# Kernel tuning notes

Hardware: AMD Instinct MI355X
Metric: run time of the kernel (lower is better)

The kernel has to match this reference:

```python
import jax, jax.numpy as jnp
import numpy as np

B, A, H, V, L = 8192, 128, 256, 64, 20


def setup_inputs() -> dict:
    key = jax.random.key(0)
    ks = jax.random.split(key, 9)
    s = lambda k, sh: jax.random.normal(k, sh, dtype=jnp.float32) * 0.05
    return {
        "attrVector": jax.random.normal(ks[0], (B, A), dtype=jnp.float32),
        "W_a": s(ks[1], (H, A)), "b_a": s(ks[2], (H,)),
        "W_ih": s(ks[3], (4 * H, V)), "W_hh": s(ks[4], (4 * H, H)),
        "b_ih": s(ks[5], (4 * H,)), "b_hh": s(ks[6], (4 * H,)),
        "W_v": s(ks[7], (V, H)), "b_v": s(ks[8], (V,)),
    }


def _lstm_step(x, h, c, W_ih, W_hh, b_ih, b_hh):
    # PyTorch LSTM gate order: input, forget, cell(g), output
    gates = x @ W_ih.T + b_ih + h @ W_hh.T + b_hh  # [B, 4H]
    i, f, g, o = jnp.split(gates, 4, axis=-1)
    c_new = jax.nn.sigmoid(f) * c + jax.nn.sigmoid(i) * jnp.tanh(g)
    h_new = jax.nn.sigmoid(o) * jnp.tanh(c_new)
    return h_new, c_new


def reference(attrVector, W_a, b_a, W_ih, W_hh, b_ih, b_hh, W_v, b_v):
    batch = attrVector.shape[0]
    dt = attrVector.dtype
    # attr2hidden -> initial hidden state; cell state zeros (init_hidden)
    h = attrVector @ W_a.T + b_a                      # [B, H]
    c = jnp.zeros_like(h)
    # start-token step (all-zeros embedding)
    x0 = jnp.zeros((batch, V), dtype=dt)
    h, c = _lstm_step(x0, h, c, W_ih, W_hh, b_ih, b_hh)

    keys = jax.random.split(jax.random.key(42), L)

    def step(carry, k):
        h, c, slp, plp, ep = carry
        logits = h @ W_v.T + b_v                      # [B, V]
        logp = jax.nn.log_softmax(logits, axis=-1)
        plp = plp + jnp.sum(jnp.exp(logp) * logp, axis=-1)  # negative entropy
        ch = jax.random.categorical(k, logits, axis=-1)     # [B] int sample
        lp = jnp.take_along_axis(logp, ch[:, None], axis=-1)[:, 0]
        slp = slp + lp
        ep = ep * jnp.exp(lp)
        x = jax.nn.one_hot(ch, V, dtype=dt)
        h2, c2 = _lstm_step(x, h, c, W_ih, W_hh, b_ih, b_hh)
        return (h2, c2, slp, plp, ep), ch

    zeros = jnp.zeros((batch,), dtype=dt)
    ones = jnp.ones((batch,), dtype=dt)
    (_, _, slp, plp, ep), msgs = jax.lax.scan(step, (h, c, zeros, zeros, ones), keys)
    message = msgs.T.astype(jnp.int64) if msgs.dtype != jnp.int64 else msgs.T  # [B, L]
    return message, slp, plp, ep
```

## Files before the change

kernel.cpp:

```cpp
#include <hip/hip_runtime.h>
#include <stdint.h>

#define BATCH 8192
#define ADIM 128
#define HDIM 256
#define VDIM 64
#define NSTEP 20
#define TB 16
#define HSP 17
#define ASP 20

typedef union { float4 v; float f[4]; } F4;

__device__ __forceinline__ uint32_t rotl32(uint32_t x, uint32_t d) {
  return (x << d) | (x >> (32u - d));
}
__device__ __forceinline__ void tf4(uint32_t& x0, uint32_t& x1, int r0, int r1, int r2, int r3) {
  x0 += x1; x1 = rotl32(x1, r0); x1 ^= x0;
  x0 += x1; x1 = rotl32(x1, r1); x1 ^= x0;
  x0 += x1; x1 = rotl32(x1, r2); x1 ^= x0;
  x0 += x1; x1 = rotl32(x1, r3); x1 ^= x0;
}
__device__ __forceinline__ void threefry2x32(uint32_t k0, uint32_t k1, uint32_t x0, uint32_t x1,
                                             uint32_t& o0, uint32_t& o1) {
  uint32_t k2 = k0 ^ k1 ^ 0x1BD11BDAu;
  x0 += k0; x1 += k1;
  tf4(x0, x1, 13, 15, 26, 6);  x0 += k1; x1 += k2 + 1u;
  tf4(x0, x1, 17, 29, 16, 24); x0 += k2; x1 += k0 + 2u;
  tf4(x0, x1, 13, 15, 26, 6);  x0 += k0; x1 += k1 + 3u;
  tf4(x0, x1, 17, 29, 16, 24); x0 += k1; x1 += k2 + 4u;
  tf4(x0, x1, 13, 15, 26, 6);  x0 += k2; x1 += k0 + 5u;
  o0 = x0; o1 = x1;
}

__device__ __forceinline__ float sigm(float x) { return 1.0f / (1.0f + expf(-x)); }

__device__ __forceinline__ float bcast(float x, int t) {
  return __int_as_float(__builtin_amdgcn_readlane(__float_as_int(x), t));
}

__global__ void prep_kernel(const float* __restrict__ Whh, const float* __restrict__ Wv,
                            const float* __restrict__ Wa, const float* __restrict__ Wih,
                            float* __restrict__ ws) {
  int n = blockIdx.x * blockDim.x + threadIdx.x;
  int stride = gridDim.x * blockDim.x;
  float* WhhT4 = ws;
  float* WvT   = ws + 262144;
  float* WaT   = ws + 278528;
  float* WihT4 = ws + 311296;
  for (int i = n; i < 256 * 1024; i += stride) {
    int k = i >> 10, rem = i & 1023, u = rem >> 2, g = rem & 3;
    WhhT4[i] = Whh[((g << 8) + u) * 256 + k];
  }
  for (int i = n; i < 256 * 64; i += stride) { int k = i >> 6, v = i & 63; WvT[i] = Wv[v * 256 + k]; }
  for (int i = n; i < 128 * 256; i += stride) { int k = i >> 8, u = i & 255; WaT[i] = Wa[u * 128 + k]; }
  for (int i = n; i < 64 * 1024; i += stride) {
    int v = i >> 10, rem = i & 1023, u = rem >> 2, g = rem & 3;
    WihT4[i] = Wih[((g << 8) + u) * 64 + v];
  }
}

__global__ __launch_bounds__(256, 2) void sender_main(
    const float* __restrict__ attr, const float* __restrict__ b_a,
    const float* __restrict__ b_ih, const float* __restrict__ b_hh,
    const float* __restrict__ b_v,
    const float* __restrict__ WhhT4, const float* __restrict__ WvT,
    const float* __restrict__ WaT, const float* __restrict__ WihT4,
    float* __restrict__ out) {
  __shared__ float h_s[HDIM][HSP];
  __shared__ __align__(16) float attr_s[ADIM][ASP];
  __shared__ float slp_s[TB], plp_s[TB], ep_s[TB];
  __shared__ int ch_s[TB];

  const int tid = threadIdx.x;
  const int w = tid >> 6;
  const int lane = tid & 63;
  const int u = (w << 6) + lane;
  const int w4 = w << 2;
  const int b0 = blockIdx.x * TB;

  if (tid < TB) { slp_s[tid] = 0.0f; plp_s[tid] = 0.0f; ep_s[tid] = 1.0f; }

  {
    int r = tid >> 5;
    int cm = (tid & 31) << 2;
    #pragma unroll
    for (int pass = 0; pass < 2; ++pass) {
      int row = r + (pass << 3);
      F4 vv; vv.v = *(const float4*)&attr[(size_t)(b0 + row) * ADIM + cm];
      attr_s[cm + 0][row] = vv.f[0];
      attr_s[cm + 1][row] = vv.f[1];
      attr_s[cm + 2][row] = vv.f[2];
      attr_s[cm + 3][row] = vv.f[3];
    }
  }
  __syncthreads();

  {
    float acc[16];
    #pragma unroll
    for (int s = 0; s < 16; ++s) acc[s] = 0.0f;
    #pragma unroll 2
    for (int k = 0; k < ADIM; ++k) {
      F4 a0, a1, a2, a3;
      a0.v = *(const float4*)&attr_s[k][0];
      a1.v = *(const float4*)&attr_s[k][4];
      a2.v = *(const float4*)&attr_s[k][8];
      a3.v = *(const float4*)&attr_s[k][12];
      float wa = WaT[(k << 8) + u];
      #pragma unroll
      for (int j = 0; j < 4; ++j) {
        acc[j]      = fmaf(a0.f[j], wa, acc[j]);
        acc[4 + j]  = fmaf(a1.f[j], wa, acc[4 + j]);
        acc[8 + j]  = fmaf(a2.f[j], wa, acc[8 + j]);
        acc[12 + j] = fmaf(a3.f[j], wa, acc[12 + j]);
      }
    }
    float ba = b_a[u];
    #pragma unroll
    for (int s = 0; s < 16; ++s) h_s[u][s] = acc[s] + ba;
  }
  __syncthreads();

  float c_r[16];
  #pragma unroll
  for (int s = 0; s < 16; ++s) c_r[s] = 0.0f;

  float bg[4];
  #pragma unroll
  for (int g = 0; g < 4; ++g) bg[g] = b_ih[(g << 8) + u] + b_hh[(g << 8) + u];
  const float bv = b_v[lane];

  {
    float ga[16][4];
    #pragma unroll
    for (int s = 0; s < 16; ++s)
      #pragma unroll
      for (int g = 0; g < 4; ++g) ga[s][g] = 0.0f;
    #pragma unroll 1
    for (int kc = 0; kc < 16; ++kc) {
      const int k0 = kc << 4;
      const int kk = k0 + (lane & 15);
      float hch[16];
      #pragma unroll
      for (int s = 0; s < 16; ++s) hch[s] = h_s[kk][(s + w4) & 15];
      #pragma unroll
      for (int t = 0; t < 16; ++t) {
        const int k = k0 + t;
        F4 wv4; wv4.v = *(const float4*)&WhhT4[(k << 10) + (u << 2)];
        #pragma unroll
        for (int s = 0; s < 16; ++s) {
          float hb = bcast(hch[s], t);
          ga[s][0] = fmaf(hb, wv4.f[0], ga[s][0]);
          ga[s][1] = fmaf(hb, wv4.f[1], ga[s][1]);
          ga[s][2] = fmaf(hb, wv4.f[2], ga[s][2]);
          ga[s][3] = fmaf(hb, wv4.f[3], ga[s][3]);
        }
      }
    }
    __syncthreads();
    float hn[16];
    #pragma unroll
    for (int s = 0; s < 16; ++s) {
      float gi = ga[s][0] + bg[0];
      float gf = ga[s][1] + bg[1];
      float gg = ga[s][2] + bg[2];
      float go = ga[s][3] + bg[3];
      float cn = sigm(gf) * c_r[s] + sigm(gi) * tanhf(gg);
      hn[s] = sigm(go) * tanhf(cn);
      c_r[s] = cn;
    }
    #pragma unroll
    for (int s = 0; s < 16; ++s) h_s[u][(s + w4) & 15] = hn[s];
    __syncthreads();
  }

  #pragma unroll 1
  for (int l = 0; l < NSTEP; ++l) {
    uint32_t kl0, kl1;
    threefry2x32(0u, 42u, 0u, (uint32_t)l, kl0, kl1);

    const bool last = (l == NSTEP - 1);
    float la[4] = {0.0f, 0.0f, 0.0f, 0.0f};
    float ga[16][4];
    #pragma unroll
    for (int s = 0; s < 16; ++s)
      #pragma unroll
      for (int g = 0; g < 4; ++g) ga[s][g] = 0.0f;

    if (!last) {
      #pragma unroll 1
      for (int kc = 0; kc < 16; ++kc) {
        const int k0 = kc << 4;
        const int kk = k0 + (lane & 15);
        float hch[16];
        #pragma unroll
        for (int s = 0; s < 16; ++s) hch[s] = h_s[kk][(s + w4) & 15];
        #pragma unroll
        for (int t = 0; t < 16; ++t) {
          const int k = k0 + t;
          F4 wv4; wv4.v = *(const float4*)&WhhT4[(k << 10) + (u << 2)];
          float wvv = WvT[(k << 6) | lane];
          #pragma unroll
          for (int s = 0; s < 16; ++s) {
            float hb = bcast(hch[s], t);
            if (s < 4) la[s] = fmaf(hb, wvv, la[s]);
            ga[s][0] = fmaf(hb, wv4.f[0], ga[s][0]);
            ga[s][1] = fmaf(hb, wv4.f[1], ga[s][1]);
            ga[s][2] = fmaf(hb, wv4.f[2], ga[s][2]);
            ga[s][3] = fmaf(hb, wv4.f[3], ga[s][3]);
          }
        }
      }
    } else {
      #pragma unroll 1
      for (int kc = 0; kc < 16; ++kc) {
        const int k0 = kc << 4;
        const int kk = k0 + (lane & 15);
        float hch[4];
        #pragma unroll
        for (int s = 0; s < 4; ++s) hch[s] = h_s[kk][(s + w4) & 15];
        #pragma unroll
        for (int t = 0; t < 16; ++t) {
          const int k = k0 + t;
          float wvv = WvT[(k << 6) | lane];
          #pragma unroll
          for (int s = 0; s < 4; ++s) la[s] = fmaf(bcast(hch[s], t), wvv, la[s]);
        }
      }
    }

    #pragma unroll
    for (int db = 0; db < 4; ++db) {
      float x = la[db] + bv;
      float m = x;
      #pragma unroll
      for (int o = 32; o > 0; o >>= 1) m = fmaxf(m, __shfl_xor(m, o));
      float e = expf(x - m);
      float s = e;
      #pragma unroll
      for (int o = 32; o > 0; o >>= 1) s += __shfl_xor(s, o);
      float lse = logf(s);
      float logp = x - m - lse;
      float p = expf(logp);
      float pe = p * logp;
      #pragma unroll
      for (int o = 32; o > 0; o >>= 1) pe += __shfl_xor(pe, o);
      uint32_t idx = ((uint32_t)(b0 + w4 + db) << 6) | (uint32_t)lane;
      uint32_t r0, r1;
      threefry2x32(kl0, kl1, 0u, idx, r0, r1);
      uint32_t bits = r0 ^ r1;
      float f01 = __uint_as_float((bits >> 9) | 0x3f800000u) - 1.0f;
      const float TINY = 1.17549435e-38f;
      float uu2 = fmaxf(TINY, f01 + TINY);
      float gn = -logf(-logf(uu2));
      float y = gn + x;
      float by = y; int bi = lane;
      #pragma unroll
      for (int o = 32; o > 0; o >>= 1) {
        float oy = __shfl_xor(by, o);
        int oi = __shfl_xor(bi, o);
        if (oy > by || (oy == by && oi < bi)) { by = oy; bi = oi; }
      }
      float lp = __shfl(logp, bi, 64);
      if (lane == 0) {
        int bb = w4 + db;
        ch_s[bb] = bi;
        slp_s[bb] += lp;
        plp_s[bb] += pe;
        ep_s[bb] *= expf(lp);
        out[(size_t)(b0 + bb) * NSTEP + l] = (float)bi;
      }
    }

    if (!last) {
      __syncthreads();
      float hn[16];
      #pragma unroll
      for (int s = 0; s < 16; ++s) {
        const int sp = (s + w4) & 15;
        F4 wi; wi.v = *(const float4*)&WihT4[(ch_s[sp] << 10) + (u << 2)];
        float gi = ga[s][0] + wi.f[0] + bg[0];
        float gf = ga[s][1] + wi.f[1] + bg[1];
        float gg = ga[s][2] + wi.f[2] + bg[2];
        float go = ga[s][3] + wi.f[3] + bg[3];
        float cn = sigm(gf) * c_r[s] + sigm(gi) * tanhf(gg);
        hn[s] = sigm(go) * tanhf(cn);
        c_r[s] = cn;
      }
      #pragma unroll
      for (int s = 0; s < 16; ++s) h_s[u][(s + w4) & 15] = hn[s];
      __syncthreads();
    }
  }

  __syncthreads();
  if (tid < TB) {
    int bb = b0 + tid;
    out[(size_t)BATCH * NSTEP + bb]             = slp_s[tid];
    out[(size_t)BATCH * NSTEP + BATCH + bb]     = plp_s[tid];
    out[(size_t)BATCH * NSTEP + 2 * BATCH + bb] = ep_s[tid];
  }
}

extern "C" void kernel_launch(void* const* d_in, const int* in_sizes, int n_in,
                              void* d_out, int out_size, void* d_ws, size_t ws_size,
                              hipStream_t stream) {
  const float* attr = (const float*)d_in[0];
  const float* W_a  = (const float*)d_in[1];
  const float* b_a  = (const float*)d_in[2];
  const float* W_ih = (const float*)d_in[3];
  const float* W_hh = (const float*)d_in[4];
  const float* b_ih = (const float*)d_in[5];
  const float* b_hh = (const float*)d_in[6];
  const float* W_v  = (const float*)d_in[7];
  const float* b_v  = (const float*)d_in[8];
  float* ws = (float*)d_ws;

  prep_kernel<<<256, 256, 0, stream>>>(W_hh, W_v, W_a, W_ih, ws);
  sender_main<<<BATCH / TB, 256, 0, stream>>>(
      attr, b_a, b_ih, b_hh, b_v,
      ws, ws + 262144, ws + 278528, ws + 311296,
      (float*)d_out);
}
```

Baseline: 1.441 ms.

## Retile LSTM gate work so each lane computes two hidden units over eight samples

The per-wave split changes from 64 hidden units × 16 samples to 128 hidden units (two per lane) × 8 samples. This halves the LDS reads of h and the cross-lane broadcasts per FMA group, which were a large share of the inner-loop cost. In exchange, each block now reads W_hh and W_ih from global/L2 twice as often, since two waves share each weight column. The rotated sample ordering keeps the logit samples aligned with the existing w4 mapping.

```diff
diff --git a/kernel.cpp b/kernel.cpp
--- a/kernel.cpp
+++ b/kernel.cpp
@@ -75,7 +75,12 @@
   const int tid = threadIdx.x;
   const int w = tid >> 6;
   const int lane = tid & 63;
-  const int u = (w << 6) + lane;
+  const int half = w & 1;
+  const int sh = w >> 1;
+  const int u_a = (half << 7) + lane;
+  const int u_b = u_a + 64;
+  const int base = sh << 3;
+  const int rot = half << 2;
   const int w4 = w << 2;
   const int b0 = blockIdx.x * TB;
 
@@ -97,81 +102,108 @@
   __syncthreads();
 
   {
-    float acc[16];
-    #pragma unroll
-    for (int s = 0; s < 16; ++s) acc[s] = 0.0f;
+    float acc[2][8];
+    #pragma unroll
+    for (int c = 0; c < 2; ++c)
+      #pragma unroll
+      for (int p = 0; p < 8; ++p) acc[c][p] = 0.0f;
     #pragma unroll 2
     for (int k = 0; k < ADIM; ++k) {
-      F4 a0, a1, a2, a3;
-      a0.v = *(const float4*)&attr_s[k][0];
-      a1.v = *(const float4*)&attr_s[k][4];
-      a2.v = *(const float4*)&attr_s[k][8];
-      a3.v = *(const float4*)&attr_s[k][12];
-      float wa = WaT[(k << 8) + u];
-      #pragma unroll
-      for (int j = 0; j < 4; ++j) {
-        acc[j]      = fmaf(a0.f[j], wa, acc[j]);
-        acc[4 + j]  = fmaf(a1.f[j], wa, acc[4 + j]);
-        acc[8 + j]  = fmaf(a2.f[j], wa, acc[8 + j]);
-        acc[12 + j] = fmaf(a3.f[j], wa, acc[12 + j]);
-      }
-    }
-    float ba = b_a[u];
-    #pragma unroll
-    for (int s = 0; s < 16; ++s) h_s[u][s] = acc[s] + ba;
+      F4 lo, hi;
+      lo.v = *(const float4*)&attr_s[k][base];
+      hi.v = *(const float4*)&attr_s[k][base + 4];
+      float wa_a = WaT[(k << 8) + u_a];
+      float wa_b = WaT[(k << 8) + u_b];
+      #pragma unroll
+      for (int p = 0; p < 8; ++p) {
+        float av = (p < 4) ? lo.f[p] : hi.f[p - 4];
+        acc[0][p] = fmaf(av, wa_a, acc[0][p]);
+        acc[1][p] = fmaf(av, wa_b, acc[1][p]);
+      }
+    }
+    float ba_a = b_a[u_a], ba_b = b_a[u_b];
+    #pragma unroll
+    for (int p = 0; p < 8; ++p) {
+      h_s[u_a][base + p] = acc[0][p] + ba_a;
+      h_s[u_b][base + p] = acc[1][p] + ba_b;
+    }
   }
   __syncthreads();
 
-  float c_r[16];
+  float c_r[2][8];
   #pragma unroll
-  for (int s = 0; s < 16; ++s) c_r[s] = 0.0f;
-
-  float bg[4];
+  for (int c = 0; c < 2; ++c)
+    #pragma unroll
+    for (int s = 0; s < 8; ++s) c_r[c][s] = 0.0f;
+
+  float bga[4], bgb[4];
   #pragma unroll
-  for (int g = 0; g < 4; ++g) bg[g] = b_ih[(g << 8) + u] + b_hh[(g << 8) + u];
+  for (int g = 0; g < 4; ++g) {
+    bga[g] = b_ih[(g << 8) + u_a] + b_hh[(g << 8) + u_a];
+    bgb[g] = b_ih[(g << 8) + u_b] + b_hh[(g << 8) + u_b];
+  }
   const float bv = b_v[lane];
 
   {
-    float ga[16][4];
-    #pragma unroll
-    for (int s = 0; s < 16; ++s)
-      #pragma unroll
-      for (int g = 0; g < 4; ++g) ga[s][g] = 0.0f;
+    float ga[2][8][4];
+    #pragma unroll
+    for (int c = 0; c < 2; ++c)
+      #pragma unroll
+      for (int s = 0; s < 8; ++s)
+        #pragma unroll
+        for (int g = 0; g < 4; ++g) ga[c][s][g] = 0.0f;
     #pragma unroll 1
     for (int kc = 0; kc < 16; ++kc) {
       const int k0 = kc << 4;
       const int kk = k0 + (lane & 15);
-      float hch[16];
-      #pragma unroll
-      for (int s = 0; s < 16; ++s) hch[s] = h_s[kk][(s + w4) & 15];
+      float hch[8];
+      #pragma unroll
+      for (int s = 0; s < 8; ++s) hch[s] = h_s[kk][base + ((s + rot) & 7)];
       #pragma unroll
       for (int t = 0; t < 16; ++t) {
         const int k = k0 + t;
-        F4 wv4; wv4.v = *(const float4*)&WhhT4[(k << 10) + (u << 2)];
-        #pragma unroll
-        for (int s = 0; s < 16; ++s) {
+        F4 wa, wb;
+        wa.v = *(const float4*)&WhhT4[(k << 10) + (u_a << 2)];
+        wb.v = *(const float4*)&WhhT4[(k << 10) + (u_b << 2)];
+        #pragma unroll
+        for (int s = 0; s < 8; ++s) {
           float hb = bcast(hch[s], t);
-          ga[s][0] = fmaf(hb, wv4.f[0], ga[s][0]);
-          ga[s][1] = fmaf(hb, wv4.f[1], ga[s][1]);
-          ga[s][2] = fmaf(hb, wv4.f[2], ga[s][2]);
-          ga[s][3] = fmaf(hb, wv4.f[3], ga[s][3]);
+          ga[0][s][0] = fmaf(hb, wa.f[0], ga[0][s][0]);
+          ga[0][s][1] = fmaf(hb, wa.f[1], ga[0][s][1]);
+          ga[0][s][2] = fmaf(hb, wa.f[2], ga[0][s][2]);
+          ga[0][s][3] = fmaf(hb, wa.f[3], ga[0][s][3]);
+          ga[1][s][0] = fmaf(hb, wb.f[0], ga[1][s][0]);
+          ga[1][s][1] = fmaf(hb, wb.f[1], ga[1][s][1]);
+          ga[1][s][2] = fmaf(hb, wb.f[2], ga[1][s][2]);
+          ga[1][s][3] = fmaf(hb, wb.f[3], ga[1][s][3]);
         }
       }
     }
     __syncthreads();
-    float hn[16];
-    #pragma unroll
-    for (int s = 0; s < 16; ++s) {
-      float gi = ga[s][0] + bg[0];
-      float gf = ga[s][1] + bg[1];
-      float gg = ga[s][2] + bg[2];
-      float go = ga[s][3] + bg[3];
-      float cn = sigm(gf) * c_r[s] + sigm(gi) * tanhf(gg);
-      hn[s] = sigm(go) * tanhf(cn);
-      c_r[s] = cn;
-    }
-    #pragma unroll
-    for (int s = 0; s < 16; ++s) h_s[u][(s + w4) & 15] = hn[s];
+    #pragma unroll
+    for (int s = 0; s < 8; ++s) {
+      const int p = base + ((s + rot) & 7);
+      {
+        float gi = ga[0][s][0] + bga[0];
+        float gf = ga[0][s][1] + bga[1];
+        float gg = ga[0][s][2] + bga[2];
+        float go = ga[0][s][3] + bga[3];
+        float cn = sigm(gf) * c_r[0][s] + sigm(gi) * tanhf(gg);
+        float hn = sigm(go) * tanhf(cn);
+        c_r[0][s] = cn;
+        h_s[u_a][p] = hn;
+      }
+      {
+        float gi = ga[1][s][0] + bgb[0];
+        float gf = ga[1][s][1] + bgb[1];
+        float gg = ga[1][s][2] + bgb[2];
+        float go = ga[1][s][3] + bgb[3];
+        float cn = sigm(gf) * c_r[1][s] + sigm(gi) * tanhf(gg);
+        float hn = sigm(go) * tanhf(cn);
+        c_r[1][s] = cn;
+        h_s[u_b][p] = hn;
+      }
+    }
     __syncthreads();
   }
 
@@ -182,33 +214,41 @@
 
     const bool last = (l == NSTEP - 1);
     float la[4] = {0.0f, 0.0f, 0.0f, 0.0f};
-    float ga[16][4];
-    #pragma unroll
-    for (int s = 0; s < 16; ++s)
-      #pragma unroll
-      for (int g = 0; g < 4; ++g) ga[s][g] = 0.0f;
+    float ga[2][8][4];
+    #pragma unroll
+    for (int c = 0; c < 2; ++c)
+      #pragma unroll
+      for (int s = 0; s < 8; ++s)
+        #pragma unroll
+        for (int g = 0; g < 4; ++g) ga[c][s][g] = 0.0f;
 
     if (!last) {
       #pragma unroll 1
       for (int kc = 0; kc < 16; ++kc) {
         const int k0 = kc << 4;
         const int kk = k0 + (lane & 15);
-        float hch[16];
-        #pragma unroll
-        for (int s = 0; s < 16; ++s) hch[s] = h_s[kk][(s + w4) & 15];
+        float hch[8];
+        #pragma unroll
+        for (int s = 0; s < 8; ++s) hch[s] = h_s[kk][base + ((s + rot) & 7)];
         #pragma unroll
         for (int t = 0; t < 16; ++t) {
           const int k = k0 + t;
-          F4 wv4; wv4.v = *(const float4*)&WhhT4[(k << 10) + (u << 2)];
+          F4 wa, wb;
+          wa.v = *(const float4*)&WhhT4[(k << 10) + (u_a << 2)];
+          wb.v = *(const float4*)&WhhT4[(k << 10) + (u_b << 2)];
           float wvv = WvT[(k << 6) | lane];
           #pragma unroll
-          for (int s = 0; s < 16; ++s) {
+          for (int s = 0; s < 8; ++s) {
             float hb = bcast(hch[s], t);
             if (s < 4) la[s] = fmaf(hb, wvv, la[s]);
-            ga[s][0] = fmaf(hb, wv4.f[0], ga[s][0]);
-            ga[s][1] = fmaf(hb, wv4.f[1], ga[s][1]);
-            ga[s][2] = fmaf(hb, wv4.f[2], ga[s][2]);
-            ga[s][3] = fmaf(hb, wv4.f[3], ga[s][3]);
+            ga[0][s][0] = fmaf(hb, wa.f[0], ga[0][s][0]);
+            ga[0][s][1] = fmaf(hb, wa.f[1], ga[0][s][1]);
+            ga[0][s][2] = fmaf(hb, wa.f[2], ga[0][s][2]);
+            ga[0][s][3] = fmaf(hb, wa.f[3], ga[0][s][3]);
+            ga[1][s][0] = fmaf(hb, wb.f[0], ga[1][s][0]);
+            ga[1][s][1] = fmaf(hb, wb.f[1], ga[1][s][1]);
+            ga[1][s][2] = fmaf(hb, wb.f[2], ga[1][s][2]);
+            ga[1][s][3] = fmaf(hb, wb.f[3], ga[1][s][3]);
           }
         }
       }
@@ -219,7 +259,7 @@
         const int kk = k0 + (lane & 15);
         float hch[4];
         #pragma unroll
-        for (int s = 0; s < 4; ++s) hch[s] = h_s[kk][(s + w4) & 15];
+        for (int s = 0; s < 4; ++s) hch[s] = h_s[kk][base + ((s + rot) & 7)];
         #pragma unroll
         for (int t = 0; t < 16; ++t) {
           const int k = k0 + t;
@@ -275,21 +315,34 @@
 
     if (!last) {
       __syncthreads();
-      float hn[16];
-      #pragma unroll
-      for (int s = 0; s < 16; ++s) {
-        const int sp = (s + w4) & 15;
-        F4 wi; wi.v = *(const float4*)&WihT4[(ch_s[sp] << 10) + (u << 2)];
-        float gi = ga[s][0] + wi.f[0] + bg[0];
-        float gf = ga[s][1] + wi.f[1] + bg[1];
-        float gg = ga[s][2] + wi.f[2] + bg[2];
-        float go = ga[s][3] + wi.f[3] + bg[3];
-        float cn = sigm(gf) * c_r[s] + sigm(gi) * tanhf(gg);
-        hn[s] = sigm(go) * tanhf(cn);
-        c_r[s] = cn;
-      }
-      #pragma unroll
-      for (int s = 0; s < 16; ++s) h_s[u][(s + w4) & 15] = hn[s];
+      #pragma unroll
+      for (int s = 0; s < 8; ++s) {
+        const int p = base + ((s + rot) & 7);
+        const int ch = ch_s[p];
+        F4 wia, wib;
+        wia.v = *(const float4*)&WihT4[(ch << 10) + (u_a << 2)];
+        wib.v = *(const float4*)&WihT4[(ch << 10) + (u_b << 2)];
+        {
+          float gi = ga[0][s][0] + wia.f[0] + bga[0];
+          float gf = ga[0][s][1] + wia.f[1] + bga[1];
+          float gg = ga[0][s][2] + wia.f[2] + bga[2];
+          float go = ga[0][s][3] + wia.f[3] + bga[3];
+          float cn = sigm(gf) * c_r[0][s] + sigm(gi) * tanhf(gg);
+          float hn = sigm(go) * tanhf(cn);
+          c_r[0][s] = cn;
+          h_s[u_a][p] = hn;
+        }
+        {
+          float gi = ga[1][s][0] + wib.f[0] + bgb[0];
+          float gf = ga[1][s][1] + wib.f[1] + bgb[1];
+          float gg = ga[1][s][2] + wib.f[2] + bgb[2];
+          float go = ga[1][s][3] + wib.f[3] + bgb[3];
+          float cn = sigm(gf) * c_r[1][s] + sigm(gi) * tanhf(gg);
+          float hn = sigm(go) * tanhf(cn);
+          c_r[1][s] = cn;
+          h_s[u_b][p] = hn;
+        }
+      }
       __syncthreads();
     }
   }
```

Measured after the change: 2.216 ms. +53.8%, slower.
